# Kernel optimization log

Measured on AMD Instinct MI355X. Metric: run time of the kernel, lower is better.

## Reference

```python
import jax, jax.numpy as jnp
import numpy as np

B, T, D, P, C = 65536, 3, 512, 32, 10  # batch, views, x_dim, p_dim, num_classes

def setup_inputs() -> dict:
    key = jax.random.key(0)
    ks = jax.random.split(key, 6)
    return {
        "x": jax.random.normal(ks[0], (B, T, D), dtype=jnp.float32),
        "Wk": jax.random.normal(ks[1], (P, D), dtype=jnp.float32) * (1.0 / np.sqrt(D)),
        "Wv": jax.random.normal(ks[2], (P, D), dtype=jnp.float32) * (1.0 / np.sqrt(D)),
        "Wq": jax.random.normal(ks[3], (P, T * D), dtype=jnp.float32) * (1.0 / np.sqrt(T * D)),
        "Wfc": jax.random.normal(ks[4], (C, P), dtype=jnp.float32) * (1.0 / np.sqrt(P)),
        "bfc": jax.random.normal(ks[5], (C,), dtype=jnp.float32) * 0.01,
    }

def reference(x, Wk, Wv, Wq, Wfc, bfc):
    # x: [B, 3, D]. Per-sample: k_i = Wk x_i, v_i = Wv x_i, q = Wq concat(x1,x2,x3)
    k = jnp.einsum('btd,pd->btp', x, Wk)                 # [B,3,P]
    v = jnp.einsum('btd,pd->btp', x, Wv)                 # [B,3,P]
    q = jnp.einsum('bf,pf->bp', x.reshape(x.shape[0], -1), Wq)  # [B,P]
    a = jax.nn.softmax(jnp.einsum('bp,btp->bt', q, k), axis=-1)  # 3-way softmax [B,3]
    c = jnp.einsum('bt,btp->bp', a, v)                   # weighted sum [B,P]
    return c @ Wfc.T + bfc                               # [B,C]
```

## Files before the change

kernel.cpp:

```cpp
#include <hip/hip_runtime.h>


typedef __attribute__((ext_vector_type(4))) float  f32x4;
typedef __attribute__((ext_vector_type(8))) _Float16 h16x8;

#define T_VIEWS 3
#define D_DIM   512
#define P_DIM   32
#define C_DIM   10
#define NROWS   80
#define NT      5
#define KC      16
#define M_TILES 2
#define M_WAVE  (M_TILES*16)
#define WAVES_PER_BLOCK 4
#define SAMPLES_PER_BLOCK (M_WAVE*WAVES_PER_BLOCK)

__global__ void build_weights(const float* __restrict__ Wk,
                              const float* __restrict__ Wv,
                              const float* __restrict__ Wq,
                              const float* __restrict__ Wfc,
                              _Float16* __restrict__ Wf) {
    const int row = blockIdx.x;
    const int t   = row / NROWS;
    const int j   = row % NROWS;
    const int d   = threadIdx.x;
    float val;
    if (j < 32) {
        val = Wk[j * D_DIM + d];
    } else if (j < 64) {
        const int p = j - 32;
        val = Wq[p * (T_VIEWS * D_DIM) + t * D_DIM + d];
    } else if (j < 64 + C_DIM) {
        const int i = j - 64;
        float s = 0.f;
        #pragma unroll
        for (int p = 0; p < P_DIM; ++p)
            s += Wfc[i * P_DIM + p] * Wv[p * D_DIM + d];
        val = s;
    } else {
        val = 0.f;
    }
    const int n = j >> 4, col = j & 15;
    const int kc = d >> 5, r = d & 31, quad = r >> 3, jj = r & 7;
    const size_t addr = (size_t)((((t * KC + kc) * NT + n) * 64) + quad * 16 + col) * 8 + jj;
    Wf[addr] = (_Float16)val;
}

__global__ __launch_bounds__(256) void attn_fused(
        const float* __restrict__ x,
        const _Float16* __restrict__ Wf,
        const float* __restrict__ bfc,
        float* __restrict__ out) {
    const int lane = threadIdx.x & 63;
    const int wave = threadIdx.x >> 6;
    const int col  = lane & 15;
    const int quad = lane >> 4;
    const int row_base = blockIdx.x * SAMPLES_PER_BLOCK + wave * M_WAVE;

    f32x4 acc[3][M_TILES][NT];
    #pragma unroll
    for (int t = 0; t < 3; ++t)
        #pragma unroll
        for (int m = 0; m < M_TILES; ++m)
            #pragma unroll
            for (int n = 0; n < NT; ++n)
                acc[t][m][n] = (f32x4)0.f;

    const float* xbase = x + (size_t)(row_base + col) * (T_VIEWS * D_DIM) + quad * 8;

    #pragma unroll
    for (int t = 0; t < 3; ++t) {
        const _Float16* wt = Wf + (size_t)t * (KC * NT * 512) + lane * 8;
        #pragma unroll 2
        for (int kc = 0; kc < KC; ++kc) {
            h16x8 b[NT];
            #pragma unroll
            for (int n = 0; n < NT; ++n)
                b[n] = *(const h16x8*)(wt + (kc * NT + n) * 512);
            #pragma unroll
            for (int m = 0; m < M_TILES; ++m) {
                const float* xp = xbase + t * D_DIM + (size_t)m * 16 * (T_VIEWS * D_DIM) + kc * 32;
                const f32x4 x0 = __builtin_nontemporal_load((const f32x4*)xp);
                const f32x4 x1 = __builtin_nontemporal_load((const f32x4*)(xp + 4));
                h16x8 a;
                #pragma unroll
                for (int i = 0; i < 4; ++i) {
                    a[i]     = (_Float16)x0[i];
                    a[i + 4] = (_Float16)x1[i];
                }
                #pragma unroll
                for (int n = 0; n < NT; ++n)
                    acc[t][m][n] = __builtin_amdgcn_mfma_f32_16x16x32_f16(a, b[n], acc[t][m][n], 0, 0, 0);
            }
        }
    }

    const float bias = (col < C_DIM) ? bfc[col] : 0.f;

    #pragma unroll
    for (int m = 0; m < M_TILES; ++m) {
        float outv[4];
        #pragma unroll
        for (int r = 0; r < 4; ++r) {
            const float qa = acc[0][m][2][r] + acc[1][m][2][r] + acc[2][m][2][r];
            const float qb = acc[0][m][3][r] + acc[1][m][3][r] + acc[2][m][3][r];
            float s0 = qa * acc[0][m][0][r] + qb * acc[0][m][1][r];
            float s1 = qa * acc[1][m][0][r] + qb * acc[1][m][1][r];
            float s2 = qa * acc[2][m][0][r] + qb * acc[2][m][1][r];
            #pragma unroll
            for (int msk = 1; msk <= 8; msk <<= 1) {
                s0 += __shfl_xor(s0, msk, 64);
                s1 += __shfl_xor(s1, msk, 64);
                s2 += __shfl_xor(s2, msk, 64);
            }
            const float mx = fmaxf(s0, fmaxf(s1, s2));
            const float e0 = __expf(s0 - mx);
            const float e1 = __expf(s1 - mx);
            const float e2 = __expf(s2 - mx);
            const float inv = 1.f / (e0 + e1 + e2);
            outv[r] = (e0 * acc[0][m][4][r] + e1 * acc[1][m][4][r] + e2 * acc[2][m][4][r]) * inv + bias;
        }
        if (col < C_DIM) {
            const int b0 = row_base + m * 16 + quad * 4;
            #pragma unroll
            for (int r = 0; r < 4; ++r)
                out[(size_t)(b0 + r) * C_DIM + col] = outv[r];
        }
    }
}

extern "C" void kernel_launch(void* const* d_in, const int* in_sizes, int n_in,
                              void* d_out, int out_size, void* d_ws, size_t ws_size,
                              hipStream_t stream) {
    const float* x   = (const float*)d_in[0];
    const float* Wk  = (const float*)d_in[1];
    const float* Wv  = (const float*)d_in[2];
    const float* Wq  = (const float*)d_in[3];
    const float* Wfc = (const float*)d_in[4];
    const float* bfc = (const float*)d_in[5];
    _Float16* Wf = (_Float16*)d_ws;

    hipLaunchKernelGGL(build_weights, dim3(T_VIEWS * NROWS), dim3(D_DIM), 0, stream,
                       Wk, Wv, Wq, Wfc, Wf);

    const int B_TOTAL = in_sizes[0] / (T_VIEWS * D_DIM);
    const int blocks = B_TOTAL / SAMPLES_PER_BLOCK;
    hipLaunchKernelGGL(attn_fused, dim3(blocks), dim3(256), 0, stream,
                       x, Wf, bfc, (float*)d_out);
}
```

Baseline: 536.7 us.

## Use one M tile per wave with x register prefetch and higher occupancy bound

Each wave now handles 16 samples instead of 32, which halves the accumulator registers. The launch bounds now request 4 blocks per CU for higher occupancy. The x operand is software-pipelined: the next K chunk is loaded before the current MFMAs run, and the pointers advance incrementally. Weight fragments are now reused across only one M tile, so weight loads per sample double, and the grid has twice as many blocks.

Result: slower. 566.8 us (+5.6%).

```diff
diff --git a/kernel.cpp b/kernel.cpp
--- a/kernel.cpp
+++ b/kernel.cpp
@@ -11,8 +11,7 @@
 #define NROWS   80
 #define NT      5
 #define KC      16
-#define M_TILES 2
-#define M_WAVE  (M_TILES*16)
+#define M_WAVE  16
 #define WAVES_PER_BLOCK 4
 #define SAMPLES_PER_BLOCK (M_WAVE*WAVES_PER_BLOCK)
 
@@ -47,7 +46,7 @@
     Wf[addr] = (_Float16)val;
 }
 
-__global__ __launch_bounds__(256) void attn_fused(
+__global__ __launch_bounds__(256, 4) void attn_fused(
         const float* __restrict__ x,
         const _Float16* __restrict__ Wf,
         const float* __restrict__ bfc,
@@ -58,75 +57,74 @@
     const int quad = lane >> 4;
     const int row_base = blockIdx.x * SAMPLES_PER_BLOCK + wave * M_WAVE;
 
-    f32x4 acc[3][M_TILES][NT];
+    f32x4 acc[3][NT];
     #pragma unroll
     for (int t = 0; t < 3; ++t)
         #pragma unroll
-        for (int m = 0; m < M_TILES; ++m)
-            #pragma unroll
-            for (int n = 0; n < NT; ++n)
-                acc[t][m][n] = (f32x4)0.f;
+        for (int n = 0; n < NT; ++n)
+            acc[t][n] = (f32x4)0.f;
 
-    const float* xbase = x + (size_t)(row_base + col) * (T_VIEWS * D_DIM) + quad * 8;
+    const float* xp = x + (size_t)(row_base + col) * (T_VIEWS * D_DIM) + quad * 8;
+    const _Float16* wp = Wf + lane * 8;
+
+    f32x4 x0 = __builtin_nontemporal_load((const f32x4*)xp);
+    f32x4 x1 = __builtin_nontemporal_load((const f32x4*)(xp + 4));
 
     #pragma unroll
     for (int t = 0; t < 3; ++t) {
-        const _Float16* wt = Wf + (size_t)t * (KC * NT * 512) + lane * 8;
         #pragma unroll 2
         for (int kc = 0; kc < KC; ++kc) {
             h16x8 b[NT];
             #pragma unroll
             for (int n = 0; n < NT; ++n)
-                b[n] = *(const h16x8*)(wt + (kc * NT + n) * 512);
+                b[n] = *(const h16x8*)(wp + n * 512);
+            const float* xn = xp + ((t == 2) ? (kc < KC - 1 ? 32 : 0) : 32);
+            const f32x4 x0n = __builtin_nontemporal_load((const f32x4*)xn);
+            const f32x4 x1n = __builtin_nontemporal_load((const f32x4*)(xn + 4));
+            h16x8 a;
             #pragma unroll
-            for (int m = 0; m < M_TILES; ++m) {
-                const float* xp = xbase + t * D_DIM + (size_t)m * 16 * (T_VIEWS * D_DIM) + kc * 32;
-                const f32x4 x0 = __builtin_nontemporal_load((const f32x4*)xp);
-                const f32x4 x1 = __builtin_nontemporal_load((const f32x4*)(xp + 4));
-                h16x8 a;
-                #pragma unroll
-                for (int i = 0; i < 4; ++i) {
-                    a[i]     = (_Float16)x0[i];
-                    a[i + 4] = (_Float16)x1[i];
-                }
-                #pragma unroll
-                for (int n = 0; n < NT; ++n)
-                    acc[t][m][n] = __builtin_amdgcn_mfma_f32_16x16x32_f16(a, b[n], acc[t][m][n], 0, 0, 0);
+            for (int i = 0; i < 4; ++i) {
+                a[i]     = (_Float16)x0[i];
+                a[i + 4] = (_Float16)x1[i];
             }
+            #pragma unroll
+            for (int n = 0; n < NT; ++n)
+                acc[t][n] = __builtin_amdgcn_mfma_f32_16x16x32_f16(a, b[n], acc[t][n], 0, 0, 0);
+            x0 = x0n; x1 = x1n;
+            xp += 32;
+            wp += NT * 512;
         }
     }
 
     const float bias = (col < C_DIM) ? bfc[col] : 0.f;
 
+    float outv[4];
     #pragma unroll
-    for (int m = 0; m < M_TILES; ++m) {
-        float outv[4];
+    for (int r = 0; r < 4; ++r) {
+        const float qa = acc[0][2][r] + acc[1][2][r] + acc[2][2][r];
+        const float qb = acc[0][3][r] + acc[1][3][r] + acc[2][3][r];
+        float s0 = qa * acc[0][0][r] + qb * acc[0][1][r];
+        float s1 = qa * acc[1][0][r] + qb * acc[1][1][r];
+        float s2 = qa * acc[2][0][r] + qb * acc[2][1][r];
         #pragma unroll
-        for (int r = 0; r < 4; ++r) {
-            const float qa = acc[0][m][2][r] + acc[1][m][2][r] + acc[2][m][2][r];
-            const float qb = acc[0][m][3][r] + acc[1][m][3][r] + acc[2][m][3][r];
-            float s0 = qa * acc[0][m][0][r] + qb * acc[0][m][1][r];
-            float s1 = qa * acc[1][m][0][r] + qb * acc[1][m][1][r];
-            float s2 = qa * acc[2][m][0][r] + qb * acc[2][m][1][r];
-            #pragma unroll
-            for (int msk = 1; msk <= 8; msk <<= 1) {
-                s0 += __shfl_xor(s0, msk, 64);
-                s1 += __shfl_xor(s1, msk, 64);
-                s2 += __shfl_xor(s2, msk, 64);
-            }
-            const float mx = fmaxf(s0, fmaxf(s1, s2));
-            const float e0 = __expf(s0 - mx);
-            const float e1 = __expf(s1 - mx);
-            const float e2 = __expf(s2 - mx);
-            const float inv = 1.f / (e0 + e1 + e2);
-            outv[r] = (e0 * acc[0][m][4][r] + e1 * acc[1][m][4][r] + e2 * acc[2][m][4][r]) * inv + bias;
+        for (int msk = 1; msk <= 8; msk <<= 1) {
+            s0 += __shfl_xor(s0, msk, 64);
+            s1 += __shfl_xor(s1, msk, 64);
+            s2 += __shfl_xor(s2, msk, 64);
         }
-        if (col < C_DIM) {
-            const int b0 = row_base + m * 16 + quad * 4;
-            #pragma unroll
-            for (int r = 0; r < 4; ++r)
-                out[(size_t)(b0 + r) * C_DIM + col] = outv[r];
-        }
+        const float mx = fmaxf(s0, fmaxf(s1, s2));
+        const float e0 = __expf(s0 - mx);
+        const float e1 = __expf(s1 - mx);
+        const float e2 = __expf(s2 - mx);
+        const float inv = 1.f / (e0 + e1 + e2);
+        outv[r] = (e0 * acc[0][4][r] + e1 * acc[1][4][r] + e2 * acc[2][4][r]) * inv + bias;
+    }
+
+    if (col < C_DIM) {
+        const int b0 = row_base + quad * 4;
+        #pragma unroll
+        for (int r = 0; r < 4; ++r)
+            out[(size_t)(b0 + r) * C_DIM + col] = outv[r];
     }
 }
 
```
